# Optimization experiments

Measured on AMD Instinct MI355X. Metric: run time of the kernel, lower is better.

## Reference

```python
import jax, jax.numpy as jnp
import numpy as np

N = 50000      # nodes
E = 800000     # edges (avg degree 16)
F_IN = 128     # num_node_features
H = 128        # hidden_channels


def setup_inputs() -> dict:
    key = jax.random.key(0)
    ks = jax.random.split(key, 9)
    x = jax.random.normal(ks[0], (N, F_IN), jnp.float32)
    edge_index = jax.random.randint(ks[1], (2, E), 0, N, dtype=jnp.int64)
    s_in = 1.0 / np.sqrt(F_IN)
    s_h = 1.0 / np.sqrt(H)
    return {
        "x": x,
        "edge_index": edge_index,
        "W1": jax.random.normal(ks[2], (F_IN, H), jnp.float32) * s_in,
        "b1": jax.random.normal(ks[3], (H,), jnp.float32) * 0.01,
        "W2": jax.random.normal(ks[4], (H, H), jnp.float32) * s_h,
        "b2": jax.random.normal(ks[5], (H,), jnp.float32) * 0.01,
        "W3": jax.random.normal(ks[6], (H, H), jnp.float32) * s_h,
        "b3": jax.random.normal(ks[7], (H,), jnp.float32) * 0.01,
    }


def gcn_layer(x, src_f, dst_f, dinv, W, b):
    # PyG GCNConv: out = D^-1/2 (A+I) D^-1/2 (x @ W) + b
    h = x @ W                                   # [N, H]
    coef = dinv[src_f] * dinv[dst_f]            # [E+N]
    msg = coef[:, None] * h[src_f]              # gather + scale, [E+N, H]
    agg = jax.ops.segment_sum(msg, dst_f, num_segments=x.shape[0])
    return agg + b


def reference(x, edge_index, W1, b1, W2, b2, W3, b3):
    n = x.shape[0]
    loops = jnp.arange(n, dtype=edge_index.dtype)
    src_f = jnp.concatenate([edge_index[0], loops])  # edges + self loops
    dst_f = jnp.concatenate([edge_index[1], loops])
    # degree with unit edge weights (edge_weight=None)
    deg = jax.ops.segment_sum(jnp.ones(src_f.shape[0], x.dtype), dst_f, num_segments=n)
    dinv = jnp.where(deg > 0, jax.lax.rsqrt(deg), 0.0)
    h = jax.nn.relu(gcn_layer(x, src_f, dst_f, dinv, W1, b1))
    # dropout p=0.1 is identity in eval mode
    h = jax.nn.relu(gcn_layer(h, src_f, dst_f, dinv, W2, b2))
    return gcn_layer(h, src_f, dst_f, dinv, W3, b3)
```

## Files before the change

kernel.cpp:

```cpp
#include <hip/hip_runtime.h>

#define HDIM 128
#define BM 64

typedef _Float16 half8 __attribute__((ext_vector_type(8)));
typedef _Float16 half4 __attribute__((ext_vector_type(4)));
typedef _Float16 half2v __attribute__((ext_vector_type(2)));
typedef float f32x4 __attribute__((ext_vector_type(4)));


__global__ void hist_k(const int* __restrict__ dst, int* __restrict__ cnt, int E) {
    int e = blockIdx.x * blockDim.x + threadIdx.x;
    if (e < E) atomicAdd(&cnt[dst[e]], 1);
}

__global__ void dinv_k(const int* __restrict__ cnt, float* __restrict__ dinv, int n) {
    int i = blockIdx.x * blockDim.x + threadIdx.x;
    if (i < n) dinv[i] = rsqrtf((float)(cnt[i] + 1));
}

__global__ void scanA_k(const int* __restrict__ cnt, int* __restrict__ offs,
                        int* __restrict__ bsum, int n) {
    __shared__ int s[256];
    int i = blockIdx.x * 256 + threadIdx.x;
    int v = (i < n) ? cnt[i] : 0;
    s[threadIdx.x] = v;
    __syncthreads();
    for (int d = 1; d < 256; d <<= 1) {
        int t = (threadIdx.x >= d) ? s[threadIdx.x - d] : 0;
        __syncthreads();
        s[threadIdx.x] += t;
        __syncthreads();
    }
    if (i < n) offs[i] = s[threadIdx.x] - v;
    if (threadIdx.x == 255) bsum[blockIdx.x] = s[255];
}

__global__ void scanB_k(int* __restrict__ bsum, int nb) {
    __shared__ int s[256];
    int v = (threadIdx.x < nb) ? bsum[threadIdx.x] : 0;
    s[threadIdx.x] = v;
    __syncthreads();
    for (int d = 1; d < 256; d <<= 1) {
        int t = (threadIdx.x >= d) ? s[threadIdx.x - d] : 0;
        __syncthreads();
        s[threadIdx.x] += t;
        __syncthreads();
    }
    if (threadIdx.x < nb) bsum[threadIdx.x] = s[threadIdx.x] - v;
}

__global__ void scanC_k(int* __restrict__ offs, const int* __restrict__ bsum,
                        int n, int E) {
    int i = blockIdx.x * blockDim.x + threadIdx.x;
    if (i < n) offs[i] += bsum[i >> 8];
    if (i == 0) offs[n] = E;
}

__global__ void fill_k(const int* __restrict__ src, const int* __restrict__ dst,
                       const int* __restrict__ offs, int* __restrict__ cur,
                       const float* __restrict__ dinv,
                       int* __restrict__ csrc, float* __restrict__ ccoef, int E) {
    int e = blockIdx.x * blockDim.x + threadIdx.x;
    if (e >= E) return;
    int s = src[e], d = dst[e];
    int p = offs[d] + atomicAdd(&cur[d], 1);
    csrc[p] = s;
    ccoef[p] = dinv[s] * dinv[d];
}


__global__ void cvt_x_k(const float* __restrict__ x, _Float16* __restrict__ xh, int total4) {
    int i = blockIdx.x * blockDim.x + threadIdx.x;
    if (i >= total4) return;
    float4 v = ((const float4*)x)[i];
    half4 o = { (_Float16)v.x, (_Float16)v.y, (_Float16)v.z, (_Float16)v.w };
    ((half4*)xh)[i] = o;
}

__global__ void cvt_w_k(const float* __restrict__ W, _Float16* __restrict__ Wp) {
    int i = blockIdx.x * 256 + threadIdx.x;
    int k = i >> 7, col = i & 127;
    Wp[((size_t)(k >> 3) * 128 + col) * 8 + (k & 7)] = (_Float16)W[i];
}


__global__ __launch_bounds__(256) void gemm_h(const _Float16* __restrict__ A,
                                              const _Float16* __restrict__ Wp,
                                              _Float16* __restrict__ C, int n) {
    const int lane = threadIdx.x & 63;
    const int wave = threadIdx.x >> 6;
    const int row0 = blockIdx.x * BM + wave * 16;
    const int rlo  = lane & 15;
    const int khi  = lane >> 4;

    f32x4 acc[8] = {};

#pragma unroll
    for (int s = 0; s < 4; ++s) {
        half8 a = {};
        int arow = row0 + rlo;
        if (arow < n)
            a = *(const half8*)&A[(size_t)arow * HDIM + 32 * s + 8 * khi];
        const int kb = 4 * s + khi;
#pragma unroll
        for (int c = 0; c < 8; ++c) {
            half8 b = *(const half8*)&Wp[((size_t)kb * HDIM + 16 * c + rlo) * 8];
            acc[c] = __builtin_amdgcn_mfma_f32_16x16x32_f16(a, b, acc[c], 0, 0, 0);
        }
    }

#pragma unroll
    for (int c = 0; c < 8; ++c) {
        int col = 16 * c + rlo;
#pragma unroll
        for (int r = 0; r < 4; ++r) {
            int row = row0 + khi * 4 + r;
            if (row < n) C[(size_t)row * HDIM + col] = (_Float16)acc[c][r];
        }
    }
}


__global__ __launch_bounds__(256) void agg_h(const _Float16* __restrict__ h,
                                             const int* __restrict__ offs,
                                             const int* __restrict__ csrc,
                                             const float* __restrict__ coef,
                                             const float* __restrict__ dinv,
                                             const float* __restrict__ bias,
                                             _Float16* __restrict__ out16,
                                             float* __restrict__ out32,
                                             int n, int relu) {
    int node = blockIdx.x * 4 + (threadIdx.x >> 6);
    int lane = threadIdx.x & 63;
    if (node >= n) return;

    const half2v* hp = (const half2v*)h;
    float di = dinv[node];
    float cs = di * di;
    half2v sv = hp[(size_t)node * 64 + lane];
    float ax = cs * (float)sv[0];
    float ay = cs * (float)sv[1];

    int e = offs[node];
    const int end = offs[node + 1];

    for (; e + 8 <= end; e += 8) {
        int   s[8];
        float c[8];
#pragma unroll
        for (int u = 0; u < 8; ++u) { s[u] = csrc[e + u]; c[u] = coef[e + u]; }
        half2v v[8];
#pragma unroll
        for (int u = 0; u < 8; ++u) v[u] = hp[(size_t)s[u] * 64 + lane];
#pragma unroll
        for (int u = 0; u < 8; ++u) {
            ax += c[u] * (float)v[u][0];
            ay += c[u] * (float)v[u][1];
        }
    }
    for (; e < end; ++e) {
        int sc = csrc[e];
        float c = coef[e];
        half2v v = hp[(size_t)sc * 64 + lane];
        ax += c * (float)v[0];
        ay += c * (float)v[1];
    }

    float2 b = ((const float2*)bias)[lane];
    ax += b.x; ay += b.y;
    if (relu) { ax = fmaxf(ax, 0.f); ay = fmaxf(ay, 0.f); }

    if (out16) {
        half2v o = { (_Float16)ax, (_Float16)ay };
        ((half2v*)out16)[(size_t)node * 64 + lane] = o;
    } else {
        float2 o; o.x = ax; o.y = ay;
        ((float2*)out32)[(size_t)node * 64 + lane] = o;
    }
}


extern "C" void kernel_launch(void* const* d_in, const int* in_sizes, int n_in,
                              void* d_out, int out_size, void* d_ws, size_t ws_size,
                              hipStream_t stream) {
    const float* x  = (const float*)d_in[0];
    const int*   ei = (const int*)d_in[1];
    const float* W1 = (const float*)d_in[2];
    const float* b1 = (const float*)d_in[3];
    const float* W2 = (const float*)d_in[4];
    const float* b2 = (const float*)d_in[5];
    const float* W3 = (const float*)d_in[6];
    const float* b3 = (const float*)d_in[7];
    float* out = (float*)d_out;

    const int n = in_sizes[0] / HDIM;
    const int E = in_sizes[1] / 2;
    const int* src = ei;
    const int* dst = ei + E;

    char* p = (char*)d_ws;
    auto alloc = [&](size_t bytes) {
        char* r = p;
        p += (bytes + 255) & ~(size_t)255;
        return r;
    };
    float*     dinv  = (float*)alloc((size_t)n * 4);
    int*       cnt   = (int*)  alloc((size_t)n * 4);
    int*       offs  = (int*)  alloc((size_t)(n + 1) * 4);
    int*       csrc  = (int*)  alloc((size_t)E * 4);
    float*     ccoef = (float*)alloc((size_t)E * 4);
    const int  nb    = (n + 255) / 256;
    int*       bsum  = (int*)  alloc((size_t)nb * 4);
    _Float16*  Wp1   = (_Float16*)alloc(HDIM * HDIM * 2);
    _Float16*  Wp2   = (_Float16*)alloc(HDIM * HDIM * 2);
    _Float16*  Wp3   = (_Float16*)alloc(HDIM * HDIM * 2);
    _Float16*  bufA  = (_Float16*)alloc(((size_t)n + 64) * HDIM * 2);
    _Float16*  bufG  = (_Float16*)alloc(((size_t)n + 64) * HDIM * 2);

    hipMemsetAsync(cnt, 0, (size_t)n * 4, stream);
    hist_k<<<(E + 255) / 256, 256, 0, stream>>>(dst, cnt, E);
    dinv_k<<<(n + 255) / 256, 256, 0, stream>>>(cnt, dinv, n);
    scanA_k<<<nb, 256, 0, stream>>>(cnt, offs, bsum, n);
    scanB_k<<<1, 256, 0, stream>>>(bsum, nb);
    scanC_k<<<(n + 255) / 256, 256, 0, stream>>>(offs, bsum, n, E);
    hipMemsetAsync(cnt, 0, (size_t)n * 4, stream);
    fill_k<<<(E + 255) / 256, 256, 0, stream>>>(src, dst, offs, cnt, dinv, csrc, ccoef, E);

    const int total4 = n * HDIM / 4;
    cvt_x_k<<<(total4 + 255) / 256, 256, 0, stream>>>(x, bufA, total4);
    cvt_w_k<<<64, 256, 0, stream>>>(W1, Wp1);
    cvt_w_k<<<64, 256, 0, stream>>>(W2, Wp2);
    cvt_w_k<<<64, 256, 0, stream>>>(W3, Wp3);

    const int gb = (n + BM - 1) / BM;
    const int ab = (n + 3) / 4;

    gemm_h<<<gb, 256, 0, stream>>>(bufA, Wp1, bufG, n);
    agg_h<<<ab, 256, 0, stream>>>(bufG, offs, csrc, ccoef, dinv, b1, bufA, nullptr, n, 1);
    gemm_h<<<gb, 256, 0, stream>>>(bufA, Wp2, bufG, n);
    agg_h<<<ab, 256, 0, stream>>>(bufG, offs, csrc, ccoef, dinv, b2, bufA, nullptr, n, 1);
    gemm_h<<<gb, 256, 0, stream>>>(bufA, Wp3, bufG, n);
    agg_h<<<ab, 256, 0, stream>>>(bufG, offs, csrc, ccoef, dinv, b3, nullptr, out, n, 0);
}
```

Measured before the change: 349.3 us.

## Fuse x conversion into first GEMM and factor edge coefficients out of CSR

Removes the separate fp32-to-fp16 conversion kernel for x by loading fp32 directly in a templated first GEMM and converting in registers. Drops the per-edge coefficient array: aggregation now gathers dinv[src] per edge and multiplies the sum by dinv[dst] once at the end, which cuts one CSR stream write and three reads. The trade is an extra random 4-byte gather of dinv per edge, though that 200KB array should be cache-resident.

```diff
diff --git a/kernel.cpp b/kernel.cpp
--- a/kernel.cpp
+++ b/kernel.cpp
@@ -4,7 +4,6 @@
 #define BM 64
 
 typedef _Float16 half8 __attribute__((ext_vector_type(8)));
-typedef _Float16 half4 __attribute__((ext_vector_type(4)));
 typedef _Float16 half2v __attribute__((ext_vector_type(2)));
 typedef float f32x4 __attribute__((ext_vector_type(4)));
 
@@ -59,24 +58,14 @@
 
 __global__ void fill_k(const int* __restrict__ src, const int* __restrict__ dst,
                        const int* __restrict__ offs, int* __restrict__ cur,
-                       const float* __restrict__ dinv,
-                       int* __restrict__ csrc, float* __restrict__ ccoef, int E) {
+                       int* __restrict__ csrc, int E) {
     int e = blockIdx.x * blockDim.x + threadIdx.x;
     if (e >= E) return;
     int s = src[e], d = dst[e];
     int p = offs[d] + atomicAdd(&cur[d], 1);
     csrc[p] = s;
-    ccoef[p] = dinv[s] * dinv[d];
-}
-
-
-__global__ void cvt_x_k(const float* __restrict__ x, _Float16* __restrict__ xh, int total4) {
-    int i = blockIdx.x * blockDim.x + threadIdx.x;
-    if (i >= total4) return;
-    float4 v = ((const float4*)x)[i];
-    half4 o = { (_Float16)v.x, (_Float16)v.y, (_Float16)v.z, (_Float16)v.w };
-    ((half4*)xh)[i] = o;
-}
+}
+
 
 __global__ void cvt_w_k(const float* __restrict__ W, _Float16* __restrict__ Wp) {
     int i = blockIdx.x * 256 + threadIdx.x;
@@ -85,7 +74,8 @@
 }
 
 
-__global__ __launch_bounds__(256) void gemm_h(const _Float16* __restrict__ A,
+template <bool A32>
+__global__ __launch_bounds__(256) void gemm_h(const void* __restrict__ Ain,
                                               const _Float16* __restrict__ Wp,
                                               _Float16* __restrict__ C, int n) {
     const int lane = threadIdx.x & 63;
@@ -100,8 +90,19 @@
     for (int s = 0; s < 4; ++s) {
         half8 a = {};
         int arow = row0 + rlo;
-        if (arow < n)
-            a = *(const half8*)&A[(size_t)arow * HDIM + 32 * s + 8 * khi];
+        if (arow < n) {
+            if constexpr (A32) {
+                const float* Af = (const float*)Ain;
+                const float4* p0 = (const float4*)&Af[(size_t)arow * HDIM + 32 * s + 8 * khi];
+                float4 lo = p0[0], hi = p0[1];
+                a[0] = (_Float16)lo.x; a[1] = (_Float16)lo.y;
+                a[2] = (_Float16)lo.z; a[3] = (_Float16)lo.w;
+                a[4] = (_Float16)hi.x; a[5] = (_Float16)hi.y;
+                a[6] = (_Float16)hi.z; a[7] = (_Float16)hi.w;
+            } else {
+                a = *(const half8*)&((const _Float16*)Ain)[(size_t)arow * HDIM + 32 * s + 8 * khi];
+            }
+        }
         const int kb = 4 * s + khi;
 #pragma unroll
         for (int c = 0; c < 8; ++c) {
@@ -125,7 +126,6 @@
 __global__ __launch_bounds__(256) void agg_h(const _Float16* __restrict__ h,
                                              const int* __restrict__ offs,
                                              const int* __restrict__ csrc,
-                                             const float* __restrict__ coef,
                                              const float* __restrict__ dinv,
                                              const float* __restrict__ bias,
                                              _Float16* __restrict__ out16,
@@ -137,38 +137,41 @@
 
     const half2v* hp = (const half2v*)h;
     float di = dinv[node];
-    float cs = di * di;
     half2v sv = hp[(size_t)node * 64 + lane];
-    float ax = cs * (float)sv[0];
-    float ay = cs * (float)sv[1];
+    float ax = di * (float)sv[0];
+    float ay = di * (float)sv[1];
 
     int e = offs[node];
     const int end = offs[node + 1];
 
     for (; e + 8 <= end; e += 8) {
-        int   s[8];
-        float c[8];
-#pragma unroll
-        for (int u = 0; u < 8; ++u) { s[u] = csrc[e + u]; c[u] = coef[e + u]; }
+        int s[8];
+#pragma unroll
+        for (int u = 0; u < 8; ++u) s[u] = csrc[e + u];
+        float ds[8];
         half2v v[8];
 #pragma unroll
-        for (int u = 0; u < 8; ++u) v[u] = hp[(size_t)s[u] * 64 + lane];
-#pragma unroll
         for (int u = 0; u < 8; ++u) {
-            ax += c[u] * (float)v[u][0];
-            ay += c[u] * (float)v[u][1];
+            ds[u] = dinv[s[u]];
+            v[u]  = hp[(size_t)s[u] * 64 + lane];
+        }
+#pragma unroll
+        for (int u = 0; u < 8; ++u) {
+            ax += ds[u] * (float)v[u][0];
+            ay += ds[u] * (float)v[u][1];
         }
     }
     for (; e < end; ++e) {
         int sc = csrc[e];
-        float c = coef[e];
+        float ds = dinv[sc];
         half2v v = hp[(size_t)sc * 64 + lane];
-        ax += c * (float)v[0];
-        ay += c * (float)v[1];
+        ax += ds * (float)v[0];
+        ay += ds * (float)v[1];
     }
 
     float2 b = ((const float2*)bias)[lane];
-    ax += b.x; ay += b.y;
+    ax = di * ax + b.x;
+    ay = di * ay + b.y;
     if (relu) { ax = fmaxf(ax, 0.f); ay = fmaxf(ay, 0.f); }
 
     if (out16) {
@@ -209,7 +212,6 @@
     int*       cnt   = (int*)  alloc((size_t)n * 4);
     int*       offs  = (int*)  alloc((size_t)(n + 1) * 4);
     int*       csrc  = (int*)  alloc((size_t)E * 4);
-    float*     ccoef = (float*)alloc((size_t)E * 4);
     const int  nb    = (n + 255) / 256;
     int*       bsum  = (int*)  alloc((size_t)nb * 4);
     _Float16*  Wp1   = (_Float16*)alloc(HDIM * HDIM * 2);
@@ -225,10 +227,8 @@
     scanB_k<<<1, 256, 0, stream>>>(bsum, nb);
     scanC_k<<<(n + 255) / 256, 256, 0, stream>>>(offs, bsum, n, E);
     hipMemsetAsync(cnt, 0, (size_t)n * 4, stream);
-    fill_k<<<(E + 255) / 256, 256, 0, stream>>>(src, dst, offs, cnt, dinv, csrc, ccoef, E);
-
-    const int total4 = n * HDIM / 4;
-    cvt_x_k<<<(total4 + 255) / 256, 256, 0, stream>>>(x, bufA, total4);
+    fill_k<<<(E + 255) / 256, 256, 0, stream>>>(src, dst, offs, cnt, csrc, E);
+
     cvt_w_k<<<64, 256, 0, stream>>>(W1, Wp1);
     cvt_w_k<<<64, 256, 0, stream>>>(W2, Wp2);
     cvt_w_k<<<64, 256, 0, stream>>>(W3, Wp3);
@@ -236,10 +236,10 @@
     const int gb = (n + BM - 1) / BM;
     const int ab = (n + 3) / 4;
 
-    gemm_h<<<gb, 256, 0, stream>>>(bufA, Wp1, bufG, n);
-    agg_h<<<ab, 256, 0, stream>>>(bufG, offs, csrc, ccoef, dinv, b1, bufA, nullptr, n, 1);
-    gemm_h<<<gb, 256, 0, stream>>>(bufA, Wp2, bufG, n);
-    agg_h<<<ab, 256, 0, stream>>>(bufG, offs, csrc, ccoef, dinv, b2, bufA, nullptr, n, 1);
-    gemm_h<<<gb, 256, 0, stream>>>(bufA, Wp3, bufG, n);
-    agg_h<<<ab, 256, 0, stream>>>(bufG, offs, csrc, ccoef, dinv, b3, nullptr, out, n, 0);
-}
+    gemm_h<true><<<gb, 256, 0, stream>>>(x, Wp1, bufG, n);
+    agg_h<<<ab, 256, 0, stream>>>(bufG, offs, csrc, dinv, b1, bufA, nullptr, n, 1);
+    gemm_h<false><<<gb, 256, 0, stream>>>(bufA, Wp2, bufG, n);
+    agg_h<<<ab, 256, 0, stream>>>(bufG, offs, csrc, dinv, b2, bufA, nullptr, n, 1);
+    gemm_h<false><<<gb, 256, 0, stream>>>(bufA, Wp3, bufG, n);
+    agg_h<<<ab, 256, 0, stream>>>(bufG, offs, csrc, dinv, b3, nullptr, out, n, 0);
+}
```

After: 340.5 us. -2.5%, faster.
